# Kernel tuning notes

Hardware: AMD Instinct MI355X
Metric: run time of the kernel (lower is better)

## Reference

```python
import jax, jax.numpy as jnp
import numpy as np
import math

N = 32768       # v_len * w_len
E = 262144
NFEAT = 512
NHID = 256
NCLASS = 40
DEPTH = 2
EPS = 0.1
PRUNE_FACTOR = 0.25


def setup_inputs() -> dict:
    key = jax.random.key(0)
    ks = jax.random.split(key, 8)
    x = jax.random.normal(ks[0], (N, NFEAT), jnp.float32)
    edge_index = jax.random.randint(ks[1], (2, E), 0, N, dtype=jnp.int64)
    edge_attr = jax.random.uniform(ks[2], (E,), jnp.float32)
    W_start = jax.random.normal(ks[3], (NHID, NFEAT), jnp.float32) / np.sqrt(NFEAT)
    b_start = jnp.zeros((NHID,), jnp.float32)
    # FAConv att_l/att_r are Linear(channels, 1, bias=False); one pair per layer
    att_l = jax.random.normal(ks[4], (DEPTH, NHID), jnp.float32) / np.sqrt(NHID)
    att_r = jax.random.normal(ks[5], (DEPTH, NHID), jnp.float32) / np.sqrt(NHID)
    W_end = jax.random.normal(ks[6], (NCLASS, NHID), jnp.float32) / np.sqrt(NHID)
    b_end = jnp.zeros((NCLASS,), jnp.float32)
    return {"x": x, "edge_index": edge_index, "edge_attr": edge_attr,
            "W_start": W_start, "b_start": b_start, "att_l": att_l,
            "att_r": att_r, "W_end": W_end, "b_end": b_end,
            "v_len": 1024, "w_len": 32}


def _forward(x, edge_attr, W_start, b_start, att_l, att_r, W_end, b_end,
             edge_index, v_len, w_len):
    src, dst = edge_index[0], edge_index[1]
    h = jax.nn.relu(x @ W_start.T + b_start)   # [N, nhid]
    h0 = h
    n = h.shape[0]
    top_idx = jnp.ones((n,), h.dtype)           # node keep-mask
    edge_mask = jnp.ones((edge_attr.shape[0],), h.dtype)  # subgraph() as edge mask
    col_off = jnp.arange(w_len)
    for l in range(DEPTH):
        # FAConv: out[i] = eps*h0[i] + sum_j w_ij * tanh(att_l.h[j] + att_r.h[i]) * h[j]
        al = h @ att_l[l]                       # [N]
        ar = h @ att_r[l]                       # [N]
        alpha = jnp.tanh(al[src] + ar[dst])     # [E]
        w = edge_attr * edge_mask
        msgs = h[src] * (alpha * w)[:, None]    # [E, nhid]
        agg = jax.ops.segment_sum(msgs, dst, num_segments=n)
        h = agg + EPS * h0
        # pruning: zero previously dropped nodes, rank by norm within each column
        h = h * top_idx[:, None]
        norm_h = jax.lax.stop_gradient(jnp.linalg.norm(h, axis=1)).reshape(v_len, w_len)
        order = jnp.argsort(-norm_h, axis=0)    # descending per column
        drop_from = math.ceil(v_len * (PRUNE_FACTOR / (l + 1)))
        drop_idx = order[drop_from:, :]         # rows to drop, per column
        flat_idx = (drop_idx * w_len + col_off).reshape(-1)
        top_idx = top_idx.at[flat_idx].set(0.0)
        # subgraph(): drop every edge touching a pruned node (== zero its weight)
        edge_mask = edge_mask * top_idx[src] * top_idx[dst]
        h = h * top_idx[:, None]
    out = h @ W_end.T + b_end
    return out * top_idx[:, None]


def reference(x, edge_index, edge_attr, W_start, b_start, att_l, att_r,
              W_end, b_end, v_len, w_len):
    return _forward(x, edge_attr, W_start, b_start, att_l, att_r, W_end, b_end,
                    edge_index, v_len, w_len)
```

## Files before the change

### kernel.cpp

```cpp
#include <hip/hip_runtime.h>
#include <math.h>

#define N_NODES 32768
#define E_EDGES 262144
#define NFEAT   512
#define NHID    256
#define NCLASS  40
#define EPSV    0.1f
#define VLEN    1024
#define WLEN    32
#define KEEP0   256
#define KEEP1   128
#define ELLW    64

typedef __attribute__((ext_vector_type(8)))  short bf16x8;
typedef __attribute__((ext_vector_type(4)))  float f32x4;
typedef __attribute__((ext_vector_type(16))) float f32x16;
typedef __attribute__((ext_vector_type(4)))  int   i32x4;

__device__ inline unsigned short f2bf(float f) {
    unsigned int u = __builtin_bit_cast(unsigned int, f);
    return (unsigned short)((u + 0x7FFFu + ((u >> 16) & 1u)) >> 16);
}
__device__ inline float bf2f(unsigned short h) {
    unsigned int u = ((unsigned int)h) << 16;
    return __builtin_bit_cast(float, u);
}

__device__ inline void split_pair(float a, float b, unsigned& hi, unsigned& lo) {
    unsigned ua = __builtin_bit_cast(unsigned, a);
    unsigned ub = __builtin_bit_cast(unsigned, b);
    unsigned ha = ua & 0xFFFF0000u, hb = ub & 0xFFFF0000u;
    hi = (ha >> 16) | hb;
    float la = a - __builtin_bit_cast(float, ha);
    float lb = b - __builtin_bit_cast(float, hb);
    unsigned ula = __builtin_bit_cast(unsigned, la);
    unsigned ulb = __builtin_bit_cast(unsigned, lb);
    lo = (ula >> 16) | (ulb & 0xFFFF0000u);
}

__device__ __forceinline__ void gload16(const void* g, void* l) {
    __builtin_amdgcn_global_load_lds(
        (const __attribute__((address_space(1))) unsigned int*)g,
        (__attribute__((address_space(3))) unsigned int*)l,
        16, 0, 0);
}

__global__ __launch_bounds__(256) void prep_kernel(
        float* __restrict__ top, const float* __restrict__ Ws,
        unsigned short* __restrict__ Whi, unsigned short* __restrict__ Wlo) {
    int blk = blockIdx.x;
    int tid = threadIdx.x;
    if (blk < 128) {
        top[blk * 256 + tid] = 1.0f;
    } else {
        int j = (blk - 128) * 256 + tid;
        float4 v = ((const float4*)Ws)[j];
        ushort4 hh, ll;
        hh.x = f2bf(v.x); ll.x = f2bf(v.x - bf2f(hh.x));
        hh.y = f2bf(v.y); ll.y = f2bf(v.y - bf2f(hh.y));
        hh.z = f2bf(v.z); ll.z = f2bf(v.z - bf2f(hh.z));
        hh.w = f2bf(v.w); ll.w = f2bf(v.w - bf2f(hh.w));
        ((ushort4*)Whi)[j] = hh;
        ((ushort4*)Wlo)[j] = ll;
    }
}

__global__ __launch_bounds__(512, 4) void gemm_scatter(
        const float* __restrict__ x, const unsigned short* __restrict__ Whi,
        const unsigned short* __restrict__ Wlo, const float* __restrict__ b,
        float* __restrict__ h0,
        const int* __restrict__ srcp, const int* __restrict__ dstp,
        const float* __restrict__ eattr, int* __restrict__ cur_,
        int* __restrict__ ell_src, float* __restrict__ ell_w) {
    __shared__ float          As[2][128 * 32];
    __shared__ unsigned short Bhs[2][128 * 32];
    __shared__ unsigned short Bls[2][128 * 32];

    if (blockIdx.x >= 512) {
        int e = (blockIdx.x - 512) * 512 + threadIdx.x;
        int d = dstp[e];
        int p = atomicAdd(&cur_[d], 1);
        if (p < ELLW) {
            ell_src[d * ELLW + p] = srcp[e];
            ell_w[d * ELLW + p]   = eattr[e];
        }
        return;
    }

    int tid  = threadIdx.x;
    int wid  = tid >> 6;
    int lane = tid & 63;
    int l31  = lane & 31;
    int khalf = lane >> 5;
    int wr = wid >> 1, wc = wid & 1;

    int wg = (blockIdx.x & 7) * 64 + (blockIdx.x >> 3);
    int row0 = (wg >> 1) * 128;
    int col0 = (wg & 1) * 128;

    f32x16 acc[2];
#pragma unroll
    for (int nr = 0; nr < 2; ++nr)
#pragma unroll
        for (int e = 0; e < 16; ++e) acc[nr][e] = 0.f;

    auto stage = [&](int kt, int buf) {
#pragma unroll
        for (int i = 0; i < 2; ++i) {
            int c    = wid * 2 + i;
            int d    = c * 1024 + lane * 16;
            int row  = d >> 7;
            int off  = d & 127;
            int loff = off ^ ((row & 7) << 4);
            const float* src = &x[(size_t)(row0 + row) * NFEAT + kt * 32 + (loff >> 2)];
            gload16(src, &As[buf][c * 256]);
        }
        {
            int d     = wid * 1024 + lane * 16;
            int wrow  = d >> 6;
            int slot  = (d >> 4) & 3;
            int lslot = slot ^ ((wrow >> 1) & 3);
            size_t so = (size_t)(col0 + wrow) * NFEAT + kt * 32 + lslot * 8;
            gload16(&Whi[so], &Bhs[buf][wid * 512]);
            gload16(&Wlo[so], &Bls[buf][wid * 512]);
        }
    };

    stage(0, 0);
    __syncthreads();

    for (int kt = 0; kt < NFEAT / 32; ++kt) {
        int cur = kt & 1;
        if (kt + 1 < NFEAT / 32) stage(kt + 1, cur ^ 1);

        const float*          Ab  = As[cur];
        const unsigned short* Bhb = Bhs[cur];
        const unsigned short* Blb = Bls[cur];

#pragma unroll
        for (int s = 0; s < 2; ++s) {
            int rt = wr * 32 + l31;
            const char* rowp = (const char*)(Ab + rt * 32);
            int lo0 = s * 64 + khalf * 32;
            int sw  = (rt & 7) << 4;
            f32x4 va = *(const f32x4*)(rowp + (lo0 ^ sw));
            f32x4 vb = *(const f32x4*)(rowp + ((lo0 + 16) ^ sw));
            unsigned h01, h23, h45, h67, l01, l23, l45, l67;
            split_pair(va[0], va[1], h01, l01);
            split_pair(va[2], va[3], h23, l23);
            split_pair(vb[0], vb[1], h45, l45);
            split_pair(vb[2], vb[3], h67, l67);
            i32x4 hv = {(int)h01, (int)h23, (int)h45, (int)h67};
            i32x4 lv = {(int)l01, (int)l23, (int)l45, (int)l67};
            bf16x8 ah  = __builtin_bit_cast(bf16x8, hv);
            bf16x8 alo = __builtin_bit_cast(bf16x8, lv);

            bf16x8 bh[2], bl[2];
#pragma unroll
            for (int nr = 0; nr < 2; ++nr) {
                int ct = wc * 64 + nr * 32 + l31;
                int lb = s * 32 + khalf * 16;
                int ob = lb ^ (((ct >> 1) & 3) << 4);
                bh[nr] = *(const bf16x8*)((const char*)(Bhb + ct * 32) + ob);
                bl[nr] = *(const bf16x8*)((const char*)(Blb + ct * 32) + ob);
            }
#pragma unroll
            for (int nr = 0; nr < 2; ++nr) {
                acc[nr] = __builtin_amdgcn_mfma_f32_32x32x16_bf16(ah,  bh[nr], acc[nr], 0, 0, 0);
                acc[nr] = __builtin_amdgcn_mfma_f32_32x32x16_bf16(ah,  bl[nr], acc[nr], 0, 0, 0);
                acc[nr] = __builtin_amdgcn_mfma_f32_32x32x16_bf16(alo, bh[nr], acc[nr], 0, 0, 0);
            }
        }
        __syncthreads();
    }

#pragma unroll
    for (int nr = 0; nr < 2; ++nr) {
        int col = col0 + wc * 64 + nr * 32 + l31;
        float bias = b[col];
#pragma unroll
        for (int r = 0; r < 16; ++r) {
            int rowt = (r & 3) + 8 * (r >> 2) + 4 * khalf;
            int row = row0 + wr * 32 + rowt;
            float v = acc[nr][r] + bias;
            h0[(size_t)row * NHID + col] = v > 0.f ? v : 0.f;
        }
    }
}

__global__ __launch_bounds__(256) void dots_kernel(
        const float* __restrict__ h, const float* __restrict__ attl,
        const float* __restrict__ attr_, float* __restrict__ al, float* __restrict__ ar) {
    int node = blockIdx.x * 4 + (threadIdx.x >> 6);
    int lane = threadIdx.x & 63;
    float4 hv = *(const float4*)&h[(size_t)node * NHID + lane * 4];
    float4 lv = *(const float4*)&attl[lane * 4];
    float4 rv = *(const float4*)&attr_[lane * 4];
    float sl = hv.x * lv.x + hv.y * lv.y + hv.z * lv.z + hv.w * lv.w;
    float sr = hv.x * rv.x + hv.y * rv.y + hv.z * rv.z + hv.w * rv.w;
#pragma unroll
    for (int off = 32; off; off >>= 1) {
        sl += __shfl_down(sl, off);
        sr += __shfl_down(sr, off);
    }
    if (lane == 0) { al[node] = sl; ar[node] = sr; }
}

__global__ __launch_bounds__(256) void gather_l0(
        const int* __restrict__ ell_src, const float* __restrict__ ell_w,
        const int* __restrict__ degp,
        const float* __restrict__ al0, const float* __restrict__ ar0,
        const float* __restrict__ h0,
        float* __restrict__ h_out, float* __restrict__ nrm,
        const float* __restrict__ attl1, const float* __restrict__ attr1,
        float* __restrict__ al1, float* __restrict__ ar1) {
    int node = blockIdx.x * 4 + (threadIdx.x >> 6);
    int lane = threadIdx.x & 63;
    size_t base = (size_t)node * NHID + lane * 4;
    float arn = ar0[node];
    int deg = degp[node]; if (deg > ELLW) deg = ELLW;
    int kbase = node * ELLW;
    float4 a1 = make_float4(0.f, 0.f, 0.f, 0.f);
    float4 a2 = make_float4(0.f, 0.f, 0.f, 0.f);
    float cv = 0.f; int sv = 0;
    if (lane < deg) {
        sv = ell_src[kbase + lane];
        cv = tanhf(al0[sv] + arn) * ell_w[kbase + lane];
    }
    int j = 0;
    for (; j + 7 < deg; j += 8) {
        float c0=__shfl(cv,j),   c1=__shfl(cv,j+1), c2=__shfl(cv,j+2), c3=__shfl(cv,j+3);
        float c4=__shfl(cv,j+4), c5=__shfl(cv,j+5), c6=__shfl(cv,j+6), c7=__shfl(cv,j+7);
        int   s0=__shfl(sv,j),   s1=__shfl(sv,j+1), s2=__shfl(sv,j+2), s3=__shfl(sv,j+3);
        int   s4=__shfl(sv,j+4), s5=__shfl(sv,j+5), s6=__shfl(sv,j+6), s7=__shfl(sv,j+7);
        float4 v0 = *(const float4*)&h0[(size_t)s0 * NHID + lane * 4];
        float4 v1 = *(const float4*)&h0[(size_t)s1 * NHID + lane * 4];
        float4 v2 = *(const float4*)&h0[(size_t)s2 * NHID + lane * 4];
        float4 v3 = *(const float4*)&h0[(size_t)s3 * NHID + lane * 4];
        float4 v4 = *(const float4*)&h0[(size_t)s4 * NHID + lane * 4];
        float4 v5 = *(const float4*)&h0[(size_t)s5 * NHID + lane * 4];
        float4 v6 = *(const float4*)&h0[(size_t)s6 * NHID + lane * 4];
        float4 v7 = *(const float4*)&h0[(size_t)s7 * NHID + lane * 4];
        a1.x += c0*v0.x + c1*v1.x + c2*v2.x + c3*v3.x;
        a1.y += c0*v0.y + c1*v1.y + c2*v2.y + c3*v3.y;
        a1.z += c0*v0.z + c1*v1.z + c2*v2.z + c3*v3.z;
        a1.w += c0*v0.w + c1*v1.w + c2*v2.w + c3*v3.w;
        a2.x += c4*v4.x + c5*v5.x + c6*v6.x + c7*v7.x;
        a2.y += c4*v4.y + c5*v5.y + c6*v6.y + c7*v7.y;
        a2.z += c4*v4.z + c5*v5.z + c6*v6.z + c7*v7.z;
        a2.w += c4*v4.w + c5*v5.w + c6*v6.w + c7*v7.w;
    }
    for (; j + 3 < deg; j += 4) {
        float c0=__shfl(cv,j), c1=__shfl(cv,j+1), c2=__shfl(cv,j+2), c3=__shfl(cv,j+3);
        int   s0=__shfl(sv,j), s1=__shfl(sv,j+1), s2=__shfl(sv,j+2), s3=__shfl(sv,j+3);
        float4 v0 = *(const float4*)&h0[(size_t)s0 * NHID + lane * 4];
        float4 v1 = *(const float4*)&h0[(size_t)s1 * NHID + lane * 4];
        float4 v2 = *(const float4*)&h0[(size_t)s2 * NHID + lane * 4];
        float4 v3 = *(const float4*)&h0[(size_t)s3 * NHID + lane * 4];
        a1.x += c0*v0.x + c1*v1.x + c2*v2.x + c3*v3.x;
        a1.y += c0*v0.y + c1*v1.y + c2*v2.y + c3*v3.y;
        a1.z += c0*v0.z + c1*v1.z + c2*v2.z + c3*v3.z;
        a1.w += c0*v0.w + c1*v1.w + c2*v2.w + c3*v3.w;
    }
    for (; j < deg; ++j) {
        float c = __shfl(cv, j);
        int   s = __shfl(sv, j);
        float4 v = *(const float4*)&h0[(size_t)s * NHID + lane * 4];
        a1.x += c*v.x; a1.y += c*v.y; a1.z += c*v.z; a1.w += c*v.w;
    }
    float4 z = *(const float4*)&h0[base];
    float4 v;
    v.x = a1.x + a2.x + EPSV * z.x;
    v.y = a1.y + a2.y + EPSV * z.y;
    v.z = a1.z + a2.z + EPSV * z.z;
    v.w = a1.w + a2.w + EPSV * z.w;
    *(float4*)&h_out[base] = v;
    float ss = v.x * v.x + v.y * v.y + v.z * v.z + v.w * v.w;
    float4 lv = *(const float4*)&attl1[lane * 4];
    float4 rv = *(const float4*)&attr1[lane * 4];
    float sl = v.x * lv.x + v.y * lv.y + v.z * lv.z + v.w * lv.w;
    float sr = v.x * rv.x + v.y * rv.y + v.z * rv.z + v.w * rv.w;
#pragma unroll
    for (int o = 32; o; o >>= 1) {
        ss += __shfl_down(ss, o);
        sl += __shfl_down(sl, o);
        sr += __shfl_down(sr, o);
    }
    if (lane == 0) { nrm[node] = sqrtf(ss); al1[node] = sl; ar1[node] = sr; }
}

__global__ __launch_bounds__(256) void gather_l1(
        const int* __restrict__ surv, const int* __restrict__ ell_src,
        const float* __restrict__ ell_w, const int* __restrict__ degp,
        const float* __restrict__ al1, const float* __restrict__ ar1,
        const float* __restrict__ top, const float* __restrict__ h_in,
        const float* __restrict__ h0,
        float* __restrict__ h_out, float* __restrict__ nrm) {
    int node = surv[blockIdx.x * 4 + (threadIdx.x >> 6)];
    int lane = threadIdx.x & 63;
    size_t base = (size_t)node * NHID + lane * 4;
    float arn = ar1[node];
    int deg = degp[node]; if (deg > ELLW) deg = ELLW;
    int kbase = node * ELLW;
    float4 acc = make_float4(0.f, 0.f, 0.f, 0.f);
    float cv = 0.f; int sv = 0;
    if (lane < deg) {
        sv = ell_src[kbase + lane];
        float w = ell_w[kbase + lane] * top[sv];
        cv = (w == 0.f) ? 0.f : tanhf(al1[sv] + arn) * w;
    }
    int j = 0;
    for (; j + 3 < deg; j += 4) {
        float c0 = __shfl(cv, j),     c1 = __shfl(cv, j + 1);
        float c2 = __shfl(cv, j + 2), c3 = __shfl(cv, j + 3);
        int   s0 = __shfl(sv, j),     s1 = __shfl(sv, j + 1);
        int   s2 = __shfl(sv, j + 2), s3 = __shfl(sv, j + 3);
        if (c0 != 0.f) { float4 v = *(const float4*)&h_in[(size_t)s0 * NHID + lane * 4];
            acc.x += c0 * v.x; acc.y += c0 * v.y; acc.z += c0 * v.z; acc.w += c0 * v.w; }
        if (c1 != 0.f) { float4 v = *(const float4*)&h_in[(size_t)s1 * NHID + lane * 4];
            acc.x += c1 * v.x; acc.y += c1 * v.y; acc.z += c1 * v.z; acc.w += c1 * v.w; }
        if (c2 != 0.f) { float4 v = *(const float4*)&h_in[(size_t)s2 * NHID + lane * 4];
            acc.x += c2 * v.x; acc.y += c2 * v.y; acc.z += c2 * v.z; acc.w += c2 * v.w; }
        if (c3 != 0.f) { float4 v = *(const float4*)&h_in[(size_t)s3 * NHID + lane * 4];
            acc.x += c3 * v.x; acc.y += c3 * v.y; acc.z += c3 * v.z; acc.w += c3 * v.w; }
    }
    for (; j < deg; ++j) {
        float c = __shfl(cv, j);
        if (c != 0.f) {
            int s = __shfl(sv, j);
            float4 v = *(const float4*)&h_in[(size_t)s * NHID + lane * 4];
            acc.x += c * v.x; acc.y += c * v.y; acc.z += c * v.z; acc.w += c * v.w;
        }
    }
    float4 z = *(const float4*)&h0[base];
    float4 v;
    v.x = acc.x + EPSV * z.x;
    v.y = acc.y + EPSV * z.y;
    v.z = acc.z + EPSV * z.z;
    v.w = acc.w + EPSV * z.w;
    *(float4*)&h_out[base] = v;
    float ss = v.x * v.x + v.y * v.y + v.z * v.z + v.w * v.w;
#pragma unroll
    for (int o = 32; o; o >>= 1) ss += __shfl_down(ss, o);
    if (lane == 0) nrm[node] = sqrtf(ss);
}

__global__ __launch_bounds__(256) void topk_kernel(
        const float* __restrict__ nrm_in, float* __restrict__ nrm_out,
        float* __restrict__ top, int drop_from, int* __restrict__ surv) {
    __shared__ float s[VLEN];
    int c     = blockIdx.x >> 2;
    int chunk = blockIdx.x & 3;
    int t = threadIdx.x;
    for (int r = t; r < VLEN; r += 256) s[r] = nrm_in[r * WLEN + c];
    __syncthreads();
    int r = chunk * 256 + t;
    float v = s[r];
    int cnt = 0;
#pragma unroll 8
    for (int r2 = 0; r2 < VLEN; ++r2) {
        float v2 = s[r2];
        cnt += (v2 > v) || (v2 == v && r2 < r);
    }
    int idx = r * WLEN + c;
    if (cnt >= drop_from) {
        top[idx] = 0.f;
        nrm_out[idx] = 0.f;
    } else {
        surv[c * drop_from + cnt] = idx;
    }
}

#define ASTR 40
#define OBSTR 264
__global__ __launch_bounds__(256) void out_mfma_list(
        const int* __restrict__ surv2, const float* __restrict__ h,
        const float* __restrict__ We, const float* __restrict__ be,
        float* __restrict__ out) {
    __shared__ unsigned short Bh[48 * OBSTR];
    __shared__ unsigned short Bl[48 * OBSTR];
    __shared__ unsigned short Ah[64 * ASTR];
    __shared__ unsigned short Al[64 * ASTR];
    __shared__ int sids[64];
    int tid  = threadIdx.x;
    int w    = tid >> 6;
    int lane = tid & 63;
    int m16  = lane & 15;
    int kblk = lane >> 4;

    if (tid < 64) sids[tid] = surv2[blockIdx.x * 64 + tid];

    for (int i = tid; i < 48 * 64; i += 256) {
        int r = i >> 6, k4 = i & 63;
        float4 v = (r < NCLASS) ? *(const float4*)&We[r * NHID + k4 * 4]
                                : make_float4(0.f, 0.f, 0.f, 0.f);
        ushort4 hh, ll;
        hh.x = f2bf(v.x); ll.x = f2bf(v.x - bf2f(hh.x));
        hh.y = f2bf(v.y); ll.y = f2bf(v.y - bf2f(hh.y));
        hh.z = f2bf(v.z); ll.z = f2bf(v.z - bf2f(hh.z));
        hh.w = f2bf(v.w); ll.w = f2bf(v.w - bf2f(hh.w));
        *(ushort4*)&Bh[r * OBSTR + k4 * 4] = hh;
        *(ushort4*)&Bl[r * OBSTR + k4 * 4] = ll;
    }
    __syncthreads();

    f32x4 acc[3];
#pragma unroll
    for (int nr = 0; nr < 3; ++nr)
#pragma unroll
        for (int e = 0; e < 4; ++e) acc[nr][e] = 0.f;

    for (int kt = 0; kt < NHID; kt += 32) {
#pragma unroll
        for (int i = 0; i < 2; ++i) {
            int f = tid + 256 * i;
            int row = f >> 3, k4 = f & 7;
            int node = sids[row];
            float4 v = *(const float4*)&h[(size_t)node * NHID + kt + k4 * 4];
            ushort4 hh, ll;
            hh.x = f2bf(v.x); ll.x = f2bf(v.x - bf2f(hh.x));
            hh.y = f2bf(v.y); ll.y = f2bf(v.y - bf2f(hh.y));
            hh.z = f2bf(v.z); ll.z = f2bf(v.z - bf2f(hh.z));
            hh.w = f2bf(v.w); ll.w = f2bf(v.w - bf2f(hh.w));
            *(ushort4*)&Ah[row * ASTR + k4 * 4] = hh;
            *(ushort4*)&Al[row * ASTR + k4 * 4] = ll;
        }
        __syncthreads();
        int ar_ = w * 16 + m16;
        bf16x8 ah  = *(const bf16x8*)&Ah[ar_ * ASTR + kblk * 8];
        bf16x8 alo = *(const bf16x8*)&Al[ar_ * ASTR + kblk * 8];
#pragma unroll
        for (int nr = 0; nr < 3; ++nr) {
            int br = nr * 16 + m16;
            bf16x8 bh = *(const bf16x8*)&Bh[br * OBSTR + kt + kblk * 8];
            bf16x8 bl = *(const bf16x8*)&Bl[br * OBSTR + kt + kblk * 8];
            acc[nr] = __builtin_amdgcn_mfma_f32_16x16x32_bf16(ah,  bh, acc[nr], 0, 0, 0);
            acc[nr] = __builtin_amdgcn_mfma_f32_16x16x32_bf16(ah,  bl, acc[nr], 0, 0, 0);
            acc[nr] = __builtin_amdgcn_mfma_f32_16x16x32_bf16(alo, bh, acc[nr], 0, 0, 0);
        }
        __syncthreads();
    }
#pragma unroll
    for (int nr = 0; nr < 3; ++nr) {
        int col = nr * 16 + m16;
        if (col < NCLASS) {
            float bias = be[col];
#pragma unroll
            for (int r = 0; r < 4; ++r) {
                int row = w * 16 + kblk * 4 + r;
                int node = sids[row];
                out[(size_t)node * NCLASS + col] = acc[nr][r] + bias;
            }
        }
    }
}

extern "C" void kernel_launch(void* const* d_in, const int* in_sizes, int n_in,
                              void* d_out, int out_size, void* d_ws, size_t ws_size,
                              hipStream_t stream) {
    const float* x     = (const float*)d_in[0];
    const int*   ei    = (const int*)d_in[1];
    const float* eattr = (const float*)d_in[2];
    const float* Ws    = (const float*)d_in[3];
    const float* bs    = (const float*)d_in[4];
    const float* attl  = (const float*)d_in[5];
    const float* attr_ = (const float*)d_in[6];
    const float* We    = (const float*)d_in[7];
    const float* be    = (const float*)d_in[8];
    float* out = (float*)d_out;

    char* ws = (char*)d_ws;
    const size_t HB = (size_t)N_NODES * NHID * sizeof(float);
    float* hA  = (float*)(ws);
    float* hB  = (float*)(ws + HB);
    float* h0  = (float*)(ws + 2 * HB);
    char* sm = ws + 3 * HB;
    float* al0      = (float*)(sm);               sm += 131072;
    float* ar0      = (float*)(sm);               sm += 131072;
    float* al1      = (float*)(sm);               sm += 131072;
    float* ar1      = (float*)(sm);               sm += 131072;
    float* nrm      = (float*)(sm);               sm += 131072;
    float* top      = (float*)(sm);               sm += 131072;
    int*   cur      = (int*)(sm);                 sm += 131072;
    int*   surv0    = (int*)(sm);                 sm += KEEP0 * WLEN * 4;
    int*   surv2    = (int*)(sm);                 sm += KEEP1 * WLEN * 4;
    unsigned short* Whi = (unsigned short*)(sm);  sm += NHID * NFEAT * 2;
    unsigned short* Wlo = (unsigned short*)(sm);  sm += NHID * NFEAT * 2;
    sm = (char*)(((size_t)sm + 255) & ~(size_t)255);
    int*   ell_src  = (int*)(sm);                 sm += (size_t)N_NODES * ELLW * 4;
    float* ell_w    = (float*)(sm);               sm += (size_t)N_NODES * ELLW * 4;

    const int* srcp = ei;
    const int* dstp = ei + E_EDGES;

    hipMemsetAsync(cur, 0, 131072, stream);
    hipMemsetAsync(d_out, 0, (size_t)out_size * sizeof(float), stream);

    prep_kernel<<<256, 256, 0, stream>>>(top, Ws, Whi, Wlo);

    gemm_scatter<<<512 + 512, 512, 0, stream>>>(x, Whi, Wlo, bs, h0,
                                                srcp, dstp, eattr, cur,
                                                ell_src, ell_w);

    dots_kernel<<<N_NODES / 4, 256, 0, stream>>>(h0, attl, attr_, al0, ar0);

    gather_l0<<<N_NODES / 4, 256, 0, stream>>>(ell_src, ell_w, cur,
                                               al0, ar0, h0, hA, nrm,
                                               attl + NHID, attr_ + NHID, al1, ar1);
    topk_kernel<<<WLEN * 4, 256, 0, stream>>>(nrm, nrm, top, KEEP0, surv0);

    gather_l1<<<(KEEP0 * WLEN) / 4, 256, 0, stream>>>(surv0, ell_src, ell_w, cur,
                                                      al1, ar1, top, hA, h0, hB, nrm);
    topk_kernel<<<WLEN * 4, 256, 0, stream>>>(nrm, nrm, top, KEEP1, surv2);

    out_mfma_list<<<(KEEP1 * WLEN) / 64, 256, 0, stream>>>(surv2, hB, We, be, out);
}
```

Measured before the change: 189.8 us.

## Fold memsets into prep kernel and ballot-skip zero edges in layer-1 gather

Removes the two hipMemsetAsync calls by having the prep kernel also zero the ELL cursor array and the output buffer, which cuts launch overhead. In gather_l1, a wave ballot builds a mask of nonzero edge coefficients. Groups of four edges that are all zero are skipped uniformly across the wave, and the per-edge branches inside a group become unconditional loads with fused accumulation. This can issue loads for zero-coefficient neighbours inside partially active groups, so some wasted bandwidth is traded for less divergence.

```diff
diff --git a/kernel.cpp b/kernel.cpp
--- a/kernel.cpp
+++ b/kernel.cpp
@@ -47,13 +47,17 @@
 }
 
 __global__ __launch_bounds__(256) void prep_kernel(
-        float* __restrict__ top, const float* __restrict__ Ws,
-        unsigned short* __restrict__ Whi, unsigned short* __restrict__ Wlo) {
+        float* __restrict__ top, int* __restrict__ cur,
+        const float* __restrict__ Ws,
+        unsigned short* __restrict__ Whi, unsigned short* __restrict__ Wlo,
+        float4* __restrict__ outz) {
     int blk = blockIdx.x;
     int tid = threadIdx.x;
     if (blk < 128) {
-        top[blk * 256 + tid] = 1.0f;
-    } else {
+        int i = blk * 256 + tid;
+        top[i] = 1.0f;
+        cur[i] = 0;
+    } else if (blk < 256) {
         int j = (blk - 128) * 256 + tid;
         float4 v = ((const float4*)Ws)[j];
         ushort4 hh, ll;
@@ -63,8 +67,12 @@
         hh.w = f2bf(v.w); ll.w = f2bf(v.w - bf2f(hh.w));
         ((ushort4*)Whi)[j] = hh;
         ((ushort4*)Wlo)[j] = ll;
-    }
-}
+    } else {
+        int j = (blk - 256) * 256 + tid;
+        outz[j] = make_float4(0.f, 0.f, 0.f, 0.f);
+    }
+}
+#define PREP_BLOCKS (256 + (N_NODES * NCLASS / 4) / 256)
 
 __global__ __launch_bounds__(512, 4) void gemm_scatter(
         const float* __restrict__ x, const unsigned short* __restrict__ Whi,
@@ -310,28 +318,29 @@
         float w = ell_w[kbase + lane] * top[sv];
         cv = (w == 0.f) ? 0.f : tanhf(al1[sv] + arn) * w;
     }
+    unsigned long long nzmask = __ballot(cv != 0.f);
     int j = 0;
     for (; j + 3 < deg; j += 4) {
+        if (((nzmask >> j) & 0xFull) == 0) continue;
         float c0 = __shfl(cv, j),     c1 = __shfl(cv, j + 1);
         float c2 = __shfl(cv, j + 2), c3 = __shfl(cv, j + 3);
         int   s0 = __shfl(sv, j),     s1 = __shfl(sv, j + 1);
         int   s2 = __shfl(sv, j + 2), s3 = __shfl(sv, j + 3);
-        if (c0 != 0.f) { float4 v = *(const float4*)&h_in[(size_t)s0 * NHID + lane * 4];
-            acc.x += c0 * v.x; acc.y += c0 * v.y; acc.z += c0 * v.z; acc.w += c0 * v.w; }
-        if (c1 != 0.f) { float4 v = *(const float4*)&h_in[(size_t)s1 * NHID + lane * 4];
-            acc.x += c1 * v.x; acc.y += c1 * v.y; acc.z += c1 * v.z; acc.w += c1 * v.w; }
-        if (c2 != 0.f) { float4 v = *(const float4*)&h_in[(size_t)s2 * NHID + lane * 4];
-            acc.x += c2 * v.x; acc.y += c2 * v.y; acc.z += c2 * v.z; acc.w += c2 * v.w; }
-        if (c3 != 0.f) { float4 v = *(const float4*)&h_in[(size_t)s3 * NHID + lane * 4];
-            acc.x += c3 * v.x; acc.y += c3 * v.y; acc.z += c3 * v.z; acc.w += c3 * v.w; }
+        float4 v0 = *(const float4*)&h_in[(size_t)s0 * NHID + lane * 4];
+        float4 v1 = *(const float4*)&h_in[(size_t)s1 * NHID + lane * 4];
+        float4 v2 = *(const float4*)&h_in[(size_t)s2 * NHID + lane * 4];
+        float4 v3 = *(const float4*)&h_in[(size_t)s3 * NHID + lane * 4];
+        acc.x += c0*v0.x + c1*v1.x + c2*v2.x + c3*v3.x;
+        acc.y += c0*v0.y + c1*v1.y + c2*v2.y + c3*v3.y;
+        acc.z += c0*v0.z + c1*v1.z + c2*v2.z + c3*v3.z;
+        acc.w += c0*v0.w + c1*v1.w + c2*v2.w + c3*v3.w;
     }
     for (; j < deg; ++j) {
+        if (!((nzmask >> j) & 1ull)) continue;
         float c = __shfl(cv, j);
-        if (c != 0.f) {
-            int s = __shfl(sv, j);
-            float4 v = *(const float4*)&h_in[(size_t)s * NHID + lane * 4];
-            acc.x += c * v.x; acc.y += c * v.y; acc.z += c * v.z; acc.w += c * v.w;
-        }
+        int   s = __shfl(sv, j);
+        float4 v = *(const float4*)&h_in[(size_t)s * NHID + lane * 4];
+        acc.x += c * v.x; acc.y += c * v.y; acc.z += c * v.z; acc.w += c * v.w;
     }
     float4 z = *(const float4*)&h0[base];
     float4 v;
@@ -494,10 +503,7 @@
     const int* srcp = ei;
     const int* dstp = ei + E_EDGES;
 
-    hipMemsetAsync(cur, 0, 131072, stream);
-    hipMemsetAsync(d_out, 0, (size_t)out_size * sizeof(float), stream);
-
-    prep_kernel<<<256, 256, 0, stream>>>(top, Ws, Whi, Wlo);
+    prep_kernel<<<PREP_BLOCKS, 256, 0, stream>>>(top, cur, Ws, Whi, Wlo, (float4*)out);
 
     gemm_scatter<<<512 + 512, 512, 0, stream>>>(x, Whi, Wlo, bs, h0,
                                                 srcp, dstp, eattr, cur,
```

Result: no change. 187.9 us (-1.0%).
